# Kernel optimization log

Measured on AMD Instinct MI355X. Metric: run time of the kernel, lower is better.

## Reference

```python
import jax, jax.numpy as jnp
import numpy as np

B, T, D, H = 4, 2048, 1024, 16
DK = D // H

def setup_inputs() -> dict:
    key = jax.random.key(0)
    k1, k2, k3 = jax.random.split(key, 3)
    s = 1.0 / np.sqrt(D)
    return {
        "x": jax.random.normal(k1, (B, T, D), dtype=jnp.float32),
        "W_qkv": jax.random.normal(k2, (D, 3 * D), dtype=jnp.float32) * s,
        "b_qkv": jnp.zeros((3 * D,), dtype=jnp.float32),
        "W_out": jax.random.normal(k3, (D, D), dtype=jnp.float32) * s,
        "b_out": jnp.zeros((D,), dtype=jnp.float32),
    }

def reference(x, W_qkv, b_qkv, W_out, b_out):
    Bx, Tx, C = x.shape
    qkv = x @ W_qkv + b_qkv                       # [B,T,3D]
    q, k, v = jnp.split(qkv, 3, axis=-1)
    # [B,T,D] -> [B,H,T,dk]
    def heads(t):
        return t.reshape(Bx, Tx, H, DK).transpose(0, 2, 1, 3)
    q, k, v = heads(q), heads(k), heads(v)
    scores = jnp.einsum('bhqd,bhkd->bhqk', q, k) / jnp.sqrt(jnp.float32(DK))
    causal = jnp.tril(jnp.ones((Tx, Tx), dtype=bool))  # [T,T]
    scores = jnp.where(causal[None, None], scores, -jnp.inf)
    attn = jax.nn.softmax(scores, axis=-1)        # dropout p=0 (eval)
    out = jnp.einsum('bhqk,bhkd->bhqd', attn, v)  # [B,H,T,dk]
    out = out.transpose(0, 2, 1, 3).reshape(Bx, Tx, C)
    return out @ W_out + b_out
```

## Files before the change

### kernel.cpp

```cpp
#include <hip/hip_runtime.h>
#include <hip/hip_bf16.h>
#include <stdint.h>

#define T_SEQ 2048
#define DMODEL 1024
#define NH 16
#define DKH 64
#define M_TOK 8192
#define N_QKV 3072
#define K_DIM 1024

#define ATTN_SC (0.125f * 1.44269504f)

typedef __attribute__((ext_vector_type(8))) short short8;
typedef __attribute__((ext_vector_type(4))) short short4v;
typedef __attribute__((ext_vector_type(4))) float float4v;
typedef __attribute__((ext_vector_type(2))) unsigned int uint2v;

__device__ inline short bf16_bits(float f) {
  __hip_bfloat16 h = __float2bfloat16(f);
  short s;
  __builtin_memcpy(&s, &h, 2);
  return s;
}

__device__ inline short4v pack4_bf16_fast(float a, float b, float c, float d) {
  unsigned ua = __builtin_bit_cast(unsigned, a) + 0x8000u;
  unsigned ub = __builtin_bit_cast(unsigned, b) + 0x8000u;
  unsigned uc = __builtin_bit_cast(unsigned, c) + 0x8000u;
  unsigned ud = __builtin_bit_cast(unsigned, d) + 0x8000u;
  uint2v uu = {(ua >> 16) | (ub & 0xFFFF0000u),
               (uc >> 16) | (ud & 0xFFFF0000u)};
  return __builtin_bit_cast(short4v, uu);
}

__device__ inline short4v pack4_bf16_trunc(float a, float b, float c, float d) {
  unsigned ua = __builtin_bit_cast(unsigned, a);
  unsigned ub = __builtin_bit_cast(unsigned, b);
  unsigned uc = __builtin_bit_cast(unsigned, c);
  unsigned ud = __builtin_bit_cast(unsigned, d);
  uint2v uu = {__builtin_amdgcn_perm(ub, ua, 0x07060302u),
               __builtin_amdgcn_perm(ud, uc, 0x07060302u)};
  return __builtin_bit_cast(short4v, uu);
}

__device__ inline void async_load16(const void* g, void* l) {
  __builtin_amdgcn_global_load_lds(
      (const __attribute__((address_space(1))) unsigned int*)g,
      (__attribute__((address_space(3))) unsigned int*)l,
      16, 0, 0);
}


__global__ __launch_bounds__(256) void cvt_kernel(const float* __restrict__ in,
                                                  short* __restrict__ out, int n) {
  int idx = (blockIdx.x * 256 + threadIdx.x) * 4;
  if (idx < n) {
    float4v v = *(const float4v*)(in + idx);
    short4v o;
    o[0] = bf16_bits(v[0]); o[1] = bf16_bits(v[1]);
    o[2] = bf16_bits(v[2]); o[3] = bf16_bits(v[3]);
    *(short4v*)(out + idx) = o;
  }
}

__global__ __launch_bounds__(256) void transpose_cvt(const float* __restrict__ in,
                                                     short* __restrict__ out,
                                                     int K, int N) {
  __shared__ float tile[32][33];
  int n0 = blockIdx.x * 32, k0 = blockIdx.y * 32;
  int tx = threadIdx.x, ty = threadIdx.y;
  #pragma unroll
  for (int r = ty; r < 32; r += 8)
    tile[r][tx] = in[(size_t)(k0 + r) * N + n0 + tx];
  __syncthreads();
  #pragma unroll
  for (int r = ty; r < 32; r += 8)
    out[(size_t)(n0 + r) * K + k0 + tx] = bf16_bits(tile[tx][r]);
}


template <bool CT>
__device__ __forceinline__ void gemm_core(
    const short* __restrict__ A, const short* __restrict__ Bt,
    int m0, int n0, int tid,
    short AsB[2][128 * 32], short BsB[2][128 * 32],
    float4v (&acc)[4][4]) {
  const int lane = tid & 63;
  const int wave = tid >> 6;
  const int wm = (wave >> 1) * 64;
  const int wn = (wave & 1) * 64;
  const int quad = lane >> 4;
  const int l16 = lane & 15;

  const int r0 = tid >> 2, r1 = r0 + 64;
  const int oswz = (((tid & 3) - (tid >> 3)) & 3) * 8;
  const int lo0 = wave * 512;
  const int lo1 = 2048 + wave * 512;

  const short* Ag0 = A  + (size_t)(m0 + r0) * K_DIM + oswz;
  const short* Ag1 = A  + (size_t)(m0 + r1) * K_DIM + oswz;
  const short* Bg0 = Bt + (size_t)(n0 + r0) * K_DIM + oswz;
  const short* Bg1 = Bt + (size_t)(n0 + r1) * K_DIM + oswz;

  const int sw = ((quad + (l16 >> 1)) & 3) * 8;

  async_load16(Ag0, &AsB[0][0] + lo0);
  async_load16(Ag1, &AsB[0][0] + lo1);
  async_load16(Bg0, &BsB[0][0] + lo0);
  async_load16(Bg1, &BsB[0][0] + lo1);

  const int nkt = K_DIM >> 5;
  for (int it = 0; it < nkt; ++it) {
    __builtin_amdgcn_s_waitcnt(0);
    __syncthreads();

    if (it + 1 < nkt) {
      const int kt = (it + 1) << 5;
      const int nb = (it + 1) & 1;
      async_load16(Ag0 + kt, &AsB[nb][0] + lo0);
      async_load16(Ag1 + kt, &AsB[nb][0] + lo1);
      async_load16(Bg0 + kt, &BsB[nb][0] + lo0);
      async_load16(Bg1 + kt, &BsB[nb][0] + lo1);
    }

    const short* As = &AsB[it & 1][0];
    const short* Bs = &BsB[it & 1][0];
    short8 af[4], bfr[4];
    #pragma unroll
    for (int t = 0; t < 4; ++t)
      af[t] = *(const short8*)(As + (size_t)(wm + t * 16 + l16) * 32 + sw);
    #pragma unroll
    for (int t = 0; t < 4; ++t)
      bfr[t] = *(const short8*)(Bs + (size_t)(wn + t * 16 + l16) * 32 + sw);
    #pragma unroll
    for (int i = 0; i < 4; ++i)
      #pragma unroll
      for (int j = 0; j < 4; ++j) {
        if (CT)
          acc[i][j] = __builtin_amdgcn_mfma_f32_16x16x32_bf16(bfr[j], af[i], acc[i][j], 0, 0, 0);
        else
          acc[i][j] = __builtin_amdgcn_mfma_f32_16x16x32_bf16(af[i], bfr[j], acc[i][j], 0, 0, 0);
      }
  }
}


__global__ __launch_bounds__(256) void gemm_qkv(
    const short* __restrict__ A, const short* __restrict__ Bt,
    const float* __restrict__ bias,
    short* __restrict__ Qb, short* __restrict__ Kf, short* __restrict__ Vf) {
  __shared__ __align__(16) short AsB[2][128 * 32];
  __shared__ __align__(16) short BsB[2][128 * 32];
  const int tid = threadIdx.x;
  const int lane = tid & 63;
  const int wave = tid >> 6;
  const int m0 = blockIdx.x * 128;
  const int n0 = blockIdx.y * 128;
  const int wm = (wave >> 1) * 64;
  const int wn = (wave & 1) * 64;
  const int quad = lane >> 4;
  const int l16 = lane & 15;

  float4v acc[4][4] = {};

  if (n0 < 2048) {
    gemm_core<true>(A, Bt, m0, n0, tid, AsB, BsB, acc);
    const int which = n0 >> 10;
    const float s = which ? 1.0f : ATTN_SC;
    short* dst = which ? Kf : Qb;
    #pragma unroll
    for (int tj = 0; tj < 4; ++tj) {
      const int colb = n0 + wn + tj * 16 + quad * 4;
      float4v bz = *(const float4v*)(bias + colb);
      float4v bzs = {bz[0] * s, bz[1] * s, bz[2] * s, bz[3] * s};
      const int d = colb & 1023;
      const int h = d >> 6, dkb = d & 63;
      const int h2 = dkb >> 5, qd = (dkb >> 3) & 3, w = dkb & 7;
      #pragma unroll
      for (int ti = 0; ti < 4; ++ti) {
        const int tok = m0 + wm + ti * 16 + l16;
        const int b = tok >> 11, t = tok & 2047;
        const size_t bhoff = (size_t)(b * NH + h) * (T_SEQ * DKH);
        float4v v = acc[ti][tj];
        short4v o = pack4_bf16_fast(fmaf(v[0], s, bzs[0]), fmaf(v[1], s, bzs[1]),
                                    fmaf(v[2], s, bzs[2]), fmaf(v[3], s, bzs[3]));
        size_t base = bhoff + (size_t)(t >> 6) * 4096 +
                      ((((t >> 4) & 3) * 2 + h2) * 4 + qd) * 128 + (t & 15) * 8 + w;
        *(short4v*)(dst + base) = o;
      }
    }
  } else {
    gemm_core<false>(A, Bt, m0, n0, tid, AsB, BsB, acc);
    #pragma unroll
    for (int tj = 0; tj < 4; ++tj) {
      const int col = n0 + wn + tj * 16 + l16;
      const float bz = bias[col];
      const int d = col & 1023;
      const int h = d >> 6, dk = d & 63;
      #pragma unroll
      for (int ti = 0; ti < 4; ++ti) {
        const int rbase = m0 + wm + ti * 16 + quad * 4;
        const int b = rbase >> 11, t = rbase & 2047;
        const size_t bhoff = (size_t)(b * NH + h) * (T_SEQ * DKH);
        float4v v = acc[ti][tj];
        short4v pv = pack4_bf16_fast(v[0] + bz, v[1] + bz, v[2] + bz, v[3] + bz);
        size_t off = bhoff + (size_t)(t >> 6) * 4096 +
                     ((((t >> 4) & 3) * 4 + (dk >> 4)) * 4 + ((t >> 2) & 3)) * 64 +
                     (dk & 15) * 4;
        *(short4v*)(Vf + off) = pv;
      }
    }
  }
}


__global__ __launch_bounds__(256) void gemm_out(
    const short* __restrict__ A, const short* __restrict__ Bt,
    const float* __restrict__ bias, float* __restrict__ Cout) {
  __shared__ __align__(16) short AsB[2][128 * 32];
  __shared__ __align__(16) short BsB[2][128 * 32];
  const int tid = threadIdx.x;
  const int lane = tid & 63;
  const int wave = tid >> 6;
  const int m0 = blockIdx.x * 128;
  const int n0 = blockIdx.y * 128;
  const int wm = (wave >> 1) * 64;
  const int wn = (wave & 1) * 64;
  const int quad = lane >> 4;
  const int l16 = lane & 15;

  float4v acc[4][4] = {};
  gemm_core<true>(A, Bt, m0, n0, tid, AsB, BsB, acc);

  #pragma unroll
  for (int tj = 0; tj < 4; ++tj) {
    const int colb = n0 + wn + tj * 16 + quad * 4;
    float4v bz = *(const float4v*)(bias + colb);
    #pragma unroll
    for (int ti = 0; ti < 4; ++ti) {
      const int row = m0 + wm + ti * 16 + l16;
      float4v v = acc[ti][tj];
      float4v o = {v[0] + bz[0], v[1] + bz[1], v[2] + bz[2], v[3] + bz[3]};
      *(float4v*)(Cout + (size_t)row * DMODEL + colb) = o;
    }
  }
}


template <int MASK>
__device__ __forceinline__ void attn_tile(
    const short* __restrict__ Ks, const short* __restrict__ Vs,
    const short8 aq[2][2], short4v ones,
    float4v oc[2][4], float4v lc[2],
    int dkq, int quad, int l16) {
  const int mb = dkq + quad * 4 - l16;
  #pragma unroll
  for (int c = 0; c < 4; ++c) {
    short8 b0 = *(const short8*)(Ks + (c * 2 + 0) * 512 + quad * 128 + l16 * 8);
    short8 b1 = *(const short8*)(Ks + (c * 2 + 1) * 512 + quad * 128 + l16 * 8);
    short4v vf[4];
    #pragma unroll
    for (int d = 0; d < 4; ++d)
      vf[d] = *(const short4v*)(Vs + (c * 4 + d) * 256 + quad * 64 + l16 * 4);
    #pragma unroll
    for (int qi = 0; qi < 2; ++qi) {
      float4v z = {0.f, 0.f, 0.f, 0.f};
      z = __builtin_amdgcn_mfma_f32_16x16x32_bf16(b0, aq[qi][0], z, 0, 0, 0);
      z = __builtin_amdgcn_mfma_f32_16x16x32_bf16(b1, aq[qi][1], z, 0, 0, 0);
      float p[4];
      #pragma unroll
      for (int i = 0; i < 4; ++i) {
        p[i] = __builtin_amdgcn_exp2f(z[i]);
        if (MASK && (mb + c * 16 + i - qi * 16 > 0)) p[i] = 0.f;
      }
      short4v pb = pack4_bf16_trunc(p[0], p[1], p[2], p[3]);
      lc[qi] = __builtin_amdgcn_mfma_f32_16x16x16bf16_1k(ones, pb, lc[qi], 0, 0, 0);
      #pragma unroll
      for (int d = 0; d < 4; ++d)
        oc[qi][d] = __builtin_amdgcn_mfma_f32_16x16x16bf16_1k(vf[d], pb, oc[qi][d], 0, 0, 0);
    }
  }
}

__global__ __launch_bounds__(256) void attn_kernel(const short* __restrict__ Qb,
                                                   const short* __restrict__ Kf,
                                                   const short* __restrict__ Vf,
                                                   short* __restrict__ Ao) {
  __shared__ __align__(16) short KsB[2][4096];
  __shared__ __align__(16) short VsB[2][4096];
  const int bh = blockIdx.x;
  const int y = blockIdx.y;
  const int qb = (y < 4) ? (15 - y) : (y < 8) ? (y - 4) : (y < 12) ? (19 - y) : (y - 8);
  const int tid = threadIdx.x;
  const int lane = tid & 63, wave = tid >> 6;
  const int quad = lane >> 4, l16 = lane & 15;
  const int qw0 = qb * 128 + wave * 32;
  const int nkb = 2 * qb + 2;

  const size_t bhoff = (size_t)bh * (T_SEQ * DKH);
  const short* Kg0 = Kf + bhoff;
  const short* Vg0 = Vf + bhoff;

  short8 aq[2][2];
  #pragma unroll
  for (int qi = 0; qi < 2; ++qi)
    #pragma unroll
    for (int h = 0; h < 2; ++h) {
      const int t = qw0 + qi * 16 + l16;
      aq[qi][h] = *(const short8*)(Qb + bhoff + (size_t)(t >> 6) * 4096 +
                                   ((((t >> 4) & 3) * 2 + h) * 4 + quad) * 128 + l16 * 8);
    }

  float4v oc[2][4] = {};
  float4v lc[2] = {};
  short4v ones = {0x3F80, 0x3F80, 0x3F80, 0x3F80};

  async_load16(Kg0 + tid * 8,        &KsB[0][0] + wave * 512);
  async_load16(Kg0 + 2048 + tid * 8, &KsB[0][0] + 2048 + wave * 512);
  async_load16(Vg0 + tid * 8,        &VsB[0][0] + wave * 512);
  async_load16(Vg0 + 2048 + tid * 8, &VsB[0][0] + 2048 + wave * 512);

  for (int kb = 0; kb < nkb; ++kb) {
    __builtin_amdgcn_s_waitcnt(0);
    __syncthreads();

    if (kb + 1 < nkb) {
      const int nb = (kb + 1) & 1;
      const short* Kg = Kg0 + (size_t)(kb + 1) * 4096;
      const short* Vg = Vg0 + (size_t)(kb + 1) * 4096;
      async_load16(Kg + tid * 8,        &KsB[nb][0] + wave * 512);
      async_load16(Kg + 2048 + tid * 8, &KsB[nb][0] + 2048 + wave * 512);
      async_load16(Vg + tid * 8,        &VsB[nb][0] + wave * 512);
      async_load16(Vg + 2048 + tid * 8, &VsB[nb][0] + 2048 + wave * 512);
    }

    const int dkq = kb * 64 - qw0;
    if (dkq + 63 <= 0) {
      attn_tile<0>(&KsB[kb & 1][0], &VsB[kb & 1][0], aq, ones, oc, lc, dkq, quad, l16);
    } else if (dkq <= 31) {
      attn_tile<1>(&KsB[kb & 1][0], &VsB[kb & 1][0], aq, ones, oc, lc, dkq, quad, l16);
    }
  }

  const int b = bh >> 4, h = bh & 15;
  #pragma unroll
  for (int qi = 0; qi < 2; ++qi) {
    float rl = 1.0f / lc[qi][0];
    #pragma unroll
    for (int d = 0; d < 4; ++d) {
      short4v o;
      #pragma unroll
      for (int i = 0; i < 4; ++i) o[i] = bf16_bits(oc[qi][d][i] * rl);
      int t = qw0 + qi * 16 + l16;
      *(short4v*)(Ao + (size_t)(b * T_SEQ + t) * DMODEL + h * DKH + d * 16 + quad * 4) = o;
    }
  }
}


extern "C" void kernel_launch(void* const* d_in, const int* in_sizes, int n_in,
                              void* d_out, int out_size, void* d_ws, size_t ws_size,
                              hipStream_t stream) {
  const float* x    = (const float*)d_in[0];
  const float* Wqkv = (const float*)d_in[1];
  const float* bqkv = (const float*)d_in[2];
  const float* Wout = (const float*)d_in[3];
  const float* bout = (const float*)d_in[4];
  float* out = (float*)d_out;

  char* ws = (char*)d_ws;
  short* Xb    = (short*)(ws);
  short* Wqkvt = (short*)(ws + (16ull << 20));
  short* Woutt = (short*)(ws + (22ull << 20));
  short* Qb    = (short*)(ws + (24ull << 20));
  short* Kf    = (short*)(ws + (40ull << 20));
  short* Vf    = (short*)(ws + (56ull << 20));
  short* Ao    = (short*)(ws + (72ull << 20));

  cvt_kernel<<<(M_TOK * K_DIM / 4 + 255) / 256, 256, 0, stream>>>(x, Xb, M_TOK * K_DIM);
  dim3 tb(32, 8);
  transpose_cvt<<<dim3(N_QKV / 32, K_DIM / 32), tb, 0, stream>>>(Wqkv, Wqkvt, K_DIM, N_QKV);
  transpose_cvt<<<dim3(DMODEL / 32, K_DIM / 32), tb, 0, stream>>>(Wout, Woutt, K_DIM, DMODEL);

  gemm_qkv<<<dim3(M_TOK / 128, N_QKV / 128), 256, 0, stream>>>(
      Xb, Wqkvt, bqkv, Qb, Kf, Vf);

  attn_kernel<<<dim3(64, T_SEQ / 128), 256, 0, stream>>>(Qb, Kf, Vf, Ao);

  gemm_out<<<dim3(M_TOK / 128, DMODEL / 128), 256, 0, stream>>>(
      Ao, Woutt, bout, out);
}
```

Measured before the change: 257.7 us.

## Merge prep kernels into one launch and store Q row-major

Merges the x conversion and the two weight transpose-conversions into a single prep_kernel launch indexed by block ID, removing two kernel launches and their gaps. It also changes the Q output of the QKV GEMM to a plain [bh, t, dk] row-major layout instead of the fragment-swizzled layout, and updates the attention kernel's Q loads to match. The Q scale is now applied after the bias add rather than fused via fma. The Q layout change may alter store and load coalescing in exchange for simpler addressing.

```diff
diff --git a/kernel.cpp b/kernel.cpp
--- a/kernel.cpp
+++ b/kernel.cpp
@@ -52,31 +52,39 @@
 }
 
 
-__global__ __launch_bounds__(256) void cvt_kernel(const float* __restrict__ in,
-                                                  short* __restrict__ out, int n) {
-  int idx = (blockIdx.x * 256 + threadIdx.x) * 4;
-  if (idx < n) {
-    float4v v = *(const float4v*)(in + idx);
+__global__ __launch_bounds__(256) void prep_kernel(
+    const float* __restrict__ x, const float* __restrict__ Wqkv,
+    const float* __restrict__ Wout,
+    short* __restrict__ Xb, short* __restrict__ Wqkvt, short* __restrict__ Woutt) {
+  __shared__ float tile[32][33];
+  const int blk = blockIdx.x;
+  const int tid = threadIdx.x;
+
+  if (blk < 8192) {
+    const int idx = (blk * 256 + tid) * 4;
+    float4v v = *(const float4v*)(x + idx);
     short4v o;
     o[0] = bf16_bits(v[0]); o[1] = bf16_bits(v[1]);
     o[2] = bf16_bits(v[2]); o[3] = bf16_bits(v[3]);
-    *(short4v*)(out + idx) = o;
-  }
-}
-
-__global__ __launch_bounds__(256) void transpose_cvt(const float* __restrict__ in,
-                                                     short* __restrict__ out,
-                                                     int K, int N) {
-  __shared__ float tile[32][33];
-  int n0 = blockIdx.x * 32, k0 = blockIdx.y * 32;
-  int tx = threadIdx.x, ty = threadIdx.y;
+    *(short4v*)(Xb + idx) = o;
+    return;
+  }
+
+  const float* in;
+  short* out;
+  int N, idx2;
+  if (blk < 11264) { in = Wqkv; out = Wqkvt; N = N_QKV;  idx2 = blk - 8192; }
+  else             { in = Wout; out = Woutt; N = DMODEL; idx2 = blk - 11264; }
+  const int ntiles = N >> 5;
+  const int n0 = (idx2 % ntiles) * 32, k0 = (idx2 / ntiles) * 32;
+  const int tx = tid & 31, ty = tid >> 5;
   #pragma unroll
   for (int r = ty; r < 32; r += 8)
     tile[r][tx] = in[(size_t)(k0 + r) * N + n0 + tx];
   __syncthreads();
   #pragma unroll
   for (int r = ty; r < 32; r += 8)
-    out[(size_t)(n0 + r) * K + k0 + tx] = bf16_bits(tile[tx][r]);
+    out[(size_t)(n0 + r) * K_DIM + k0 + tx] = bf16_bits(tile[tx][r]);
 }
 
 
@@ -167,27 +175,29 @@
   if (n0 < 2048) {
     gemm_core<true>(A, Bt, m0, n0, tid, AsB, BsB, acc);
     const int which = n0 >> 10;
-    const float s = which ? 1.0f : ATTN_SC;
-    short* dst = which ? Kf : Qb;
     #pragma unroll
     for (int tj = 0; tj < 4; ++tj) {
       const int colb = n0 + wn + tj * 16 + quad * 4;
       float4v bz = *(const float4v*)(bias + colb);
-      float4v bzs = {bz[0] * s, bz[1] * s, bz[2] * s, bz[3] * s};
       const int d = colb & 1023;
       const int h = d >> 6, dkb = d & 63;
-      const int h2 = dkb >> 5, qd = (dkb >> 3) & 3, w = dkb & 7;
       #pragma unroll
       for (int ti = 0; ti < 4; ++ti) {
         const int tok = m0 + wm + ti * 16 + l16;
         const int b = tok >> 11, t = tok & 2047;
         const size_t bhoff = (size_t)(b * NH + h) * (T_SEQ * DKH);
         float4v v = acc[ti][tj];
-        short4v o = pack4_bf16_fast(fmaf(v[0], s, bzs[0]), fmaf(v[1], s, bzs[1]),
-                                    fmaf(v[2], s, bzs[2]), fmaf(v[3], s, bzs[3]));
-        size_t base = bhoff + (size_t)(t >> 6) * 4096 +
-                      ((((t >> 4) & 3) * 2 + h2) * 4 + qd) * 128 + (t & 15) * 8 + w;
-        *(short4v*)(dst + base) = o;
+        if (which == 0) {
+          short4v o = pack4_bf16_fast((v[0] + bz[0]) * ATTN_SC, (v[1] + bz[1]) * ATTN_SC,
+                                      (v[2] + bz[2]) * ATTN_SC, (v[3] + bz[3]) * ATTN_SC);
+          *(short4v*)(Qb + bhoff + (size_t)t * DKH + dkb) = o;
+        } else {
+          short4v o = pack4_bf16_fast(v[0] + bz[0], v[1] + bz[1], v[2] + bz[2], v[3] + bz[3]);
+          const int h2 = dkb >> 5, qd = (dkb >> 3) & 3, w = dkb & 7;
+          size_t kbase = bhoff + (size_t)(t >> 6) * 4096 +
+                         ((((t >> 4) & 3) * 2 + h2) * 4 + qd) * 128 + (t & 15) * 8 + w;
+          *(short4v*)(Kf + kbase) = o;
+        }
       }
     }
   } else {
@@ -298,19 +308,16 @@
   const int qw0 = qb * 128 + wave * 32;
   const int nkb = 2 * qb + 2;
 
-  const size_t bhoff = (size_t)bh * (T_SEQ * DKH);
-  const short* Kg0 = Kf + bhoff;
-  const short* Vg0 = Vf + bhoff;
+  const short* Qg = Qb + ((size_t)bh * T_SEQ + qw0) * DKH;
+  const short* Kg0 = Kf + (size_t)bh * (T_SEQ * DKH);
+  const short* Vg0 = Vf + (size_t)bh * (T_SEQ * DKH);
 
   short8 aq[2][2];
   #pragma unroll
   for (int qi = 0; qi < 2; ++qi)
     #pragma unroll
-    for (int h = 0; h < 2; ++h) {
-      const int t = qw0 + qi * 16 + l16;
-      aq[qi][h] = *(const short8*)(Qb + bhoff + (size_t)(t >> 6) * 4096 +
-                                   ((((t >> 4) & 3) * 2 + h) * 4 + quad) * 128 + l16 * 8);
-    }
+    for (int h = 0; h < 2; ++h)
+      aq[qi][h] = *(const short8*)(Qg + (size_t)(qi * 16 + l16) * DKH + h * 32 + quad * 8);
 
   float4v oc[2][4] = {};
   float4v lc[2] = {};
@@ -378,10 +385,7 @@
   short* Vf    = (short*)(ws + (56ull << 20));
   short* Ao    = (short*)(ws + (72ull << 20));
 
-  cvt_kernel<<<(M_TOK * K_DIM / 4 + 255) / 256, 256, 0, stream>>>(x, Xb, M_TOK * K_DIM);
-  dim3 tb(32, 8);
-  transpose_cvt<<<dim3(N_QKV / 32, K_DIM / 32), tb, 0, stream>>>(Wqkv, Wqkvt, K_DIM, N_QKV);
-  transpose_cvt<<<dim3(DMODEL / 32, K_DIM / 32), tb, 0, stream>>>(Wout, Woutt, K_DIM, DMODEL);
+  prep_kernel<<<12288, 256, 0, stream>>>(x, Wqkv, Wout, Xb, Wqkvt, Woutt);
 
   gemm_qkv<<<dim3(M_TOK / 128, N_QKV / 128), 256, 0, stream>>>(
       Xb, Wqkvt, bqkv, Qb, Kf, Vf);
```

Result: no change. 253.3 us (-1.7%).
